# Optimization experiments

Measured on AMD Instinct MI355X. Metric: run time of the kernel, lower is better.

Reference implementation:

```python
import jax, jax.numpy as jnp
import numpy as np

MARGIN = 0.35
SCALE = 64.0
EPS = 1e-8  # torch F.cosine_similarity norm clamp


def setup_inputs() -> dict:
    key = jax.random.key(0)
    k1, k2 = jax.random.split(key)
    N, D = 8192, 512
    embeddings = jax.random.normal(k1, (N, D), dtype=jnp.float32)
    labels = jax.random.randint(k2, (N,), 0, 128, dtype=jnp.int64)
    return {"embeddings": embeddings, "labels": labels}


def reference(embeddings, labels):
    # cosine similarity as Gram matrix of norm-clamped-normalized rows
    norms = jnp.maximum(jnp.linalg.norm(embeddings, axis=1, keepdims=True), EPS)
    e = embeddings / norms                      # [N, D]
    sim = jnp.einsum('id,jd->ij', e, e)         # [N, N]
    pos_mask = (labels[:, None] == labels[None, :]).astype(sim.dtype)
    # pos_sim - neg_sim = sim*mask - sim*(1-mask) = sim*(2*mask - 1)
    signed = sim * (2.0 * pos_mask - 1.0)
    loss = jnp.log1p(jnp.exp(-SCALE * (signed - MARGIN)))
    return jnp.mean(loss)
```

## Files before the change

### kernel.cpp

```cpp
#include <hip/hip_runtime.h>


typedef unsigned short u16;
typedef unsigned int u32;
typedef __attribute__((ext_vector_type(4))) float f32x4;
typedef __attribute__((ext_vector_type(8))) short bf16x8;
typedef __attribute__((ext_vector_type(8))) u16 u16x8;

#define AS1 __attribute__((address_space(1)))
#define AS3 __attribute__((address_space(3)))

__global__ __launch_bounds__(256) void norm_bf16_k(
    const float* __restrict__ emb, u16* __restrict__ e, int N, int D) {
  const int wid = threadIdx.x >> 6, lane = threadIdx.x & 63;
  const int row = blockIdx.x * 4 + wid;
  if (row >= N) return;
  const float* p = emb + (size_t)row * D + lane * 8;
  f32x4 a = *(const f32x4*)p;
  f32x4 b = *(const f32x4*)(p + 4);
  float ss = 0.f;
#pragma unroll
  for (int i = 0; i < 4; ++i) ss += a[i] * a[i] + b[i] * b[i];
#pragma unroll
  for (int o = 32; o >= 1; o >>= 1) ss += __shfl_xor(ss, o, 64);
  const float inv = 1.0f / fmaxf(sqrtf(ss), 1e-8f);
  u16x8 hv;
#pragma unroll
  for (int i = 0; i < 8; ++i) {
    float x = (i < 4 ? a[i] : b[i - 4]) * inv;
    u32 u = __float_as_uint(x);
    u += 0x7FFFu + ((u >> 16) & 1u);
    hv[i] = (u16)(u >> 16);
  }
  *(u16x8*)(e + (size_t)row * D + lane * 8) = hv;
}

__global__ __launch_bounds__(256, 3) void gram_loss_k(
    const u16* __restrict__ e, const int* __restrict__ labels,
    float* __restrict__ partials, int N, int D, int NT, int nwg) {
  __shared__ __attribute__((aligned(16))) u16 sA[3][8 * 512];
  __shared__ __attribute__((aligned(16))) u16 sB[3][8 * 512];
  __shared__ float swred[4];

  const int tid = threadIdx.x, wid = tid >> 6, lane = tid & 63;

  const int q8 = nwg >> 3, r8 = nwg & 7;
  const int x = blockIdx.x & 7, p = blockIdx.x >> 3;
  const int bid = (x < r8 ? x * (q8 + 1) : r8 * (q8 + 1) + (x - r8) * q8) + p;

  int I = 0, rem = bid, rl = NT;
  while (rem >= rl) { rem -= rl; ++I; --rl; }
  const int J = I + rem;
  const int i0 = I * 128, j0 = J * 128;

  const int rbase = (wid < 2) ? i0 : j0;
  const int fq0 = (wid & 1) * 4;
  u32 goff[4];
#pragma unroll
  for (int qq = 0; qq < 4; ++qq)
    goff[qq] = (u32)(rbase + (fq0 + qq) * 16 + (lane & 15)) * (u32)D +
               ((lane >> 4) * 8);

  const f32x4 z = {0.f, 0.f, 0.f, 0.f};
  f32x4 acc[4][4];
#pragma unroll
  for (int m = 0; m < 4; ++m)
#pragma unroll
    for (int n = 0; n < 4; ++n) acc[m][n] = z;

  const int wr = wid >> 1, wc = wid & 1;

  auto stage = [&](int buf, int kk) {
    u16* dst = ((wid < 2) ? sA[buf] : sB[buf]) + fq0 * 512;
#pragma unroll
    for (int qq = 0; qq < 4; ++qq)
      __builtin_amdgcn_global_load_lds((const AS1 void*)(e + goff[qq] + kk),
                                       (AS3 void*)(dst + qq * 512), 16, 0, 0);
  };
  auto compute = [&](int buf) {
    bf16x8 a[4], b[4];
#pragma unroll
    for (int m = 0; m < 4; ++m)
      a[m] = *(const bf16x8*)&sA[buf][(wr * 4 + m) * 512 + lane * 8];
#pragma unroll
    for (int n = 0; n < 4; ++n)
      b[n] = *(const bf16x8*)&sB[buf][(wc * 4 + n) * 512 + lane * 8];
#pragma unroll
    for (int m = 0; m < 4; ++m)
#pragma unroll
      for (int n = 0; n < 4; ++n)
        acc[m][n] =
            __builtin_amdgcn_mfma_f32_16x16x32_bf16(a[m], b[n], acc[m][n], 0, 0, 0);
  };

  stage(0, 0);
  stage(1, 32);
  stage(2, 64);

#define STEP(T, VM)                                          \
  asm volatile("s_waitcnt vmcnt(" #VM ")" ::: "memory");     \
  __builtin_amdgcn_s_barrier();                              \
  asm volatile("" ::: "memory");                             \
  compute((T) % 3);                                          \
  __builtin_amdgcn_s_barrier();                              \
  if ((T) + 3 < 16) stage((T) % 3, ((T) + 3) * 32);

  STEP(0, 8)  STEP(1, 8)  STEP(2, 8)  STEP(3, 8)
  STEP(4, 8)  STEP(5, 8)  STEP(6, 8)  STEP(7, 8)
  STEP(8, 8)  STEP(9, 8)  STEP(10, 8) STEP(11, 8)
  STEP(12, 8) STEP(13, 8) STEP(14, 4) STEP(15, 0)
#undef STEP

  const float C0 = 64.0f * 0.35f;
  float lsum = 0.f;
  const int rb = i0 + wr * 64, cb = j0 + wc * 64;
#pragma unroll
  for (int m = 0; m < 4; ++m) {
    const int gi0 = rb + m * 16 + (lane >> 4) * 4;
#pragma unroll
    for (int n = 0; n < 4; ++n) {
      const int gj = cb + n * 16 + (lane & 15);
      const int lj = labels[gj];
#pragma unroll
      for (int r = 0; r < 4; ++r) {
        const int li = labels[gi0 + r];
        float s = acc[m][n][r];
        float sg = (li == lj) ? s : -s;
        float xv = fmaf(-64.0f, sg, C0);
        float ax = fabsf(xv);
        lsum += fmaxf(xv, 0.f) + __logf(1.0f + __expf(-ax));
      }
    }
  }

#pragma unroll
  for (int o = 32; o >= 1; o >>= 1) lsum += __shfl_xor(lsum, o, 64);
  if (lane == 0) swred[wid] = lsum;
  __syncthreads();
  if (tid == 0) {
    float t = swred[0] + swred[1] + swred[2] + swred[3];
    partials[bid] = (I == J) ? t : 2.0f * t;
  }
}

__global__ __launch_bounds__(256) void reduce_k(const float* __restrict__ partials,
                                                int n, float* __restrict__ out,
                                                double invNN) {
  double s = 0.0;
  for (int i = threadIdx.x; i < n; i += 256) s += (double)partials[i];
#pragma unroll
  for (int o = 32; o >= 1; o >>= 1) s += __shfl_xor(s, o, 64);
  __shared__ double sd[4];
  const int wid = threadIdx.x >> 6, lane = threadIdx.x & 63;
  if (lane == 0) sd[wid] = s;
  __syncthreads();
  if (threadIdx.x == 0) out[0] = (float)((sd[0] + sd[1] + sd[2] + sd[3]) * invNN);
}

extern "C" void kernel_launch(void* const* d_in, const int* in_sizes, int n_in,
                              void* d_out, int out_size, void* d_ws, size_t ws_size,
                              hipStream_t stream) {
  const float* emb = (const float*)d_in[0];
  const int* labels = (const int*)d_in[1];
  float* out = (float*)d_out;

  const int N = in_sizes[1];
  const int D = in_sizes[0] / N;
  const int NT = N / 128;
  const int nTiles = NT * (NT + 1) / 2;

  u16* e = (u16*)d_ws;
  float* partials = (float*)(e + (size_t)N * D);

  norm_bf16_k<<<N / 4, 256, 0, stream>>>(emb, e, N, D);
  gram_loss_k<<<nTiles, 256, 0, stream>>>(e, labels, partials, N, D, NT, nTiles);
  reduce_k<<<1, 256, 0, stream>>>(partials, nTiles, out,
                                  1.0 / ((double)N * (double)N));
}
```

Before: 143.4 us.

## Use 256x256 tiles with 512-thread blocks and fuse final reduction via atomics

Doubles the Gram output tile to 256x256 per workgroup with 8 waves, each computing a 128x64 sub-tile, and stages 64-wide K slices in a double buffer instead of a triple buffer of 32-wide slices. MFMA blocks are wrapped in s_setprio. The separate reduce kernel is dropped: each block atomically adds its scaled partial into the output after a memset. Larger tiles raise arithmetic intensity and cut tile count, but leave only 528 blocks (fewer waves to balance across CUs), use more LDS and registers, and make the float atomic sum order nondeterministic.

```diff
diff --git a/kernel.cpp b/kernel.cpp
--- a/kernel.cpp
+++ b/kernel.cpp
@@ -35,12 +35,11 @@
   *(u16x8*)(e + (size_t)row * D + lane * 8) = hv;
 }
 
-__global__ __launch_bounds__(256, 3) void gram_loss_k(
+__global__ __launch_bounds__(512, 2) void gram_loss_k(
     const u16* __restrict__ e, const int* __restrict__ labels,
-    float* __restrict__ partials, int N, int D, int NT, int nwg) {
-  __shared__ __attribute__((aligned(16))) u16 sA[3][8 * 512];
-  __shared__ __attribute__((aligned(16))) u16 sB[3][8 * 512];
-  __shared__ float swred[4];
+    float* __restrict__ out, int N, int D, int NT, int nwg, float invNN) {
+  __shared__ __attribute__((aligned(16))) u16 sL[2][2][32 * 512];
+  __shared__ float swred[8];
 
   const int tid = threadIdx.x, wid = tid >> 6, lane = tid & 63;
 
@@ -51,71 +50,74 @@
   int I = 0, rem = bid, rl = NT;
   while (rem >= rl) { rem -= rl; ++I; --rl; }
   const int J = I + rem;
-  const int i0 = I * 128, j0 = J * 128;
+  const int i0 = I * 256, j0 = J * 256;
 
-  const int rbase = (wid < 2) ? i0 : j0;
-  const int fq0 = (wid & 1) * 4;
-  u32 goff[4];
+  const int ab = wid >> 2;
+  const int rbase = ab ? j0 : i0;
+  const int f0 = (wid & 3) * 8;
+  u32 goff[8];
 #pragma unroll
-  for (int qq = 0; qq < 4; ++qq)
-    goff[qq] = (u32)(rbase + (fq0 + qq) * 16 + (lane & 15)) * (u32)D +
-               ((lane >> 4) * 8);
+  for (int q = 0; q < 8; ++q) {
+    const int f = f0 + q, mf = f >> 1, ks = f & 1;
+    goff[q] = (u32)(rbase + mf * 16 + (lane & 15)) * (u32)D + ks * 32 +
+              ((lane >> 4) * 8);
+  }
 
   const f32x4 z = {0.f, 0.f, 0.f, 0.f};
-  f32x4 acc[4][4];
+  f32x4 acc[8][4];
 #pragma unroll
-  for (int m = 0; m < 4; ++m)
+  for (int m = 0; m < 8; ++m)
 #pragma unroll
     for (int n = 0; n < 4; ++n) acc[m][n] = z;
 
-  const int wr = wid >> 1, wc = wid & 1;
+  const int wr = wid >> 2, wc = wid & 3;
 
   auto stage = [&](int buf, int kk) {
-    u16* dst = ((wid < 2) ? sA[buf] : sB[buf]) + fq0 * 512;
 #pragma unroll
-    for (int qq = 0; qq < 4; ++qq)
-      __builtin_amdgcn_global_load_lds((const AS1 void*)(e + goff[qq] + kk),
-                                       (AS3 void*)(dst + qq * 512), 16, 0, 0);
-  };
-  auto compute = [&](int buf) {
-    bf16x8 a[4], b[4];
-#pragma unroll
-    for (int m = 0; m < 4; ++m)
-      a[m] = *(const bf16x8*)&sA[buf][(wr * 4 + m) * 512 + lane * 8];
-#pragma unroll
-    for (int n = 0; n < 4; ++n)
-      b[n] = *(const bf16x8*)&sB[buf][(wc * 4 + n) * 512 + lane * 8];
-#pragma unroll
-    for (int m = 0; m < 4; ++m)
-#pragma unroll
-      for (int n = 0; n < 4; ++n)
-        acc[m][n] =
-            __builtin_amdgcn_mfma_f32_16x16x32_bf16(a[m], b[n], acc[m][n], 0, 0, 0);
+    for (int q = 0; q < 8; ++q)
+      __builtin_amdgcn_global_load_lds((const AS1 void*)(e + goff[q] + kk),
+                                       (AS3 void*)(&sL[buf][ab][(f0 + q) * 512]),
+                                       16, 0, 0);
   };
 
   stage(0, 0);
-  stage(1, 32);
-  stage(2, 64);
 
-#define STEP(T, VM)                                          \
-  asm volatile("s_waitcnt vmcnt(" #VM ")" ::: "memory");     \
-  __builtin_amdgcn_s_barrier();                              \
-  asm volatile("" ::: "memory");                             \
-  compute((T) % 3);                                          \
-  __builtin_amdgcn_s_barrier();                              \
-  if ((T) + 3 < 16) stage((T) % 3, ((T) + 3) * 32);
-
-  STEP(0, 8)  STEP(1, 8)  STEP(2, 8)  STEP(3, 8)
-  STEP(4, 8)  STEP(5, 8)  STEP(6, 8)  STEP(7, 8)
-  STEP(8, 8)  STEP(9, 8)  STEP(10, 8) STEP(11, 8)
-  STEP(12, 8) STEP(13, 8) STEP(14, 4) STEP(15, 0)
-#undef STEP
+#pragma unroll
+  for (int t = 0; t < 8; ++t) {
+    const int buf = t & 1;
+    asm volatile("s_waitcnt vmcnt(0)" ::: "memory");
+    __builtin_amdgcn_s_barrier();
+    if (t < 7) stage(buf ^ 1, (t + 1) * 64);
+#pragma unroll
+    for (int ks = 0; ks < 2; ++ks) {
+      bf16x8 b[4];
+#pragma unroll
+      for (int n = 0; n < 4; ++n)
+        b[n] = *(const bf16x8*)&sL[buf][1][(((wc * 4 + n) << 1) + ks) * 512 + lane * 8];
+#pragma unroll
+      for (int mh = 0; mh < 2; ++mh) {
+        bf16x8 a[4];
+#pragma unroll
+        for (int m = 0; m < 4; ++m)
+          a[m] = *(const bf16x8*)&sL[buf][0]
+                     [(((wr * 8 + mh * 4 + m) << 1) + ks) * 512 + lane * 8];
+        __builtin_amdgcn_s_setprio(1);
+#pragma unroll
+        for (int m = 0; m < 4; ++m)
+#pragma unroll
+          for (int n = 0; n < 4; ++n)
+            acc[mh * 4 + m][n] = __builtin_amdgcn_mfma_f32_16x16x32_bf16(
+                a[m], b[n], acc[mh * 4 + m][n], 0, 0, 0);
+        __builtin_amdgcn_s_setprio(0);
+      }
+    }
+  }
 
   const float C0 = 64.0f * 0.35f;
   float lsum = 0.f;
-  const int rb = i0 + wr * 64, cb = j0 + wc * 64;
+  const int rb = i0 + wr * 128, cb = j0 + wc * 64;
 #pragma unroll
-  for (int m = 0; m < 4; ++m) {
+  for (int m = 0; m < 8; ++m) {
     const int gi0 = rb + m * 16 + (lane >> 4) * 4;
 #pragma unroll
     for (int n = 0; n < 4; ++n) {
@@ -138,23 +140,12 @@
   if (lane == 0) swred[wid] = lsum;
   __syncthreads();
   if (tid == 0) {
-    float t = swred[0] + swred[1] + swred[2] + swred[3];
-    partials[bid] = (I == J) ? t : 2.0f * t;
+    float t = 0.f;
+#pragma unroll
+    for (int w = 0; w < 8; ++w) t += swred[w];
+    const float wgt = (I == J) ? 1.0f : 2.0f;
+    atomicAdd(out, t * wgt * invNN);
   }
-}
-
-__global__ __launch_bounds__(256) void reduce_k(const float* __restrict__ partials,
-                                                int n, float* __restrict__ out,
-                                                double invNN) {
-  double s = 0.0;
-  for (int i = threadIdx.x; i < n; i += 256) s += (double)partials[i];
-#pragma unroll
-  for (int o = 32; o >= 1; o >>= 1) s += __shfl_xor(s, o, 64);
-  __shared__ double sd[4];
-  const int wid = threadIdx.x >> 6, lane = threadIdx.x & 63;
-  if (lane == 0) sd[wid] = s;
-  __syncthreads();
-  if (threadIdx.x == 0) out[0] = (float)((sd[0] + sd[1] + sd[2] + sd[3]) * invNN);
 }
 
 extern "C" void kernel_launch(void* const* d_in, const int* in_sizes, int n_in,
@@ -166,14 +157,13 @@
 
   const int N = in_sizes[1];
   const int D = in_sizes[0] / N;
-  const int NT = N / 128;
+  const int NT = N / 256;
   const int nTiles = NT * (NT + 1) / 2;
 
   u16* e = (u16*)d_ws;
-  float* partials = (float*)(e + (size_t)N * D);
 
+  hipMemsetAsync(out, 0, sizeof(float), stream);
   norm_bf16_k<<<N / 4, 256, 0, stream>>>(emb, e, N, D);
-  gram_loss_k<<<nTiles, 256, 0, stream>>>(e, labels, partials, N, D, NT, nTiles);
-  reduce_k<<<1, 256, 0, stream>>>(partials, nTiles, out,
-                                  1.0 / ((double)N * (double)N));
+  gram_loss_k<<<nTiles, 512, 0, stream>>>(e, labels, out, N, D, NT, nTiles,
+                                          (float)(1.0 / ((double)N * (double)N)));
 }
```

After: 164.1 us. 1.14x slower.
